# Performance work log

Hardware: AMD Instinct MI355X
Metric: run time of the kernel (lower is better)

The kernel has to match this reference:

```python
import jax, jax.numpy as jnp
import numpy as np
from jax import lax

TEMP = 0.1  # softmax_temp default in forward


def _conv(x, w, b):
    y = lax.conv_general_dilated(x, w, (1, 1), 'VALID',
                                 dimension_numbers=('NCHW', 'OIHW', 'NCHW'))
    return y + b[None, :, None, None]


def _avg_pool2(x):
    # AvgPool2d(2,2), floor mode (VALID window)
    s = lax.reduce_window(x, 0.0, lax.add, (1, 1, 2, 2), (1, 1, 2, 2), 'VALID')
    return s / 4.0


def _cnn(x, c1w, c1b, c2w, c2b, c3w, c3b, dw, db):
    x = _avg_pool2(jax.nn.relu(_conv(x, c1w, c1b)))   # (N,8,13,13)
    x = _avg_pool2(jax.nn.relu(_conv(x, c2w, c2b)))   # (N,16,5,5)
    x = _avg_pool2(jax.nn.relu(_conv(x, c3w, c3b)))   # (N,32,1,1)
    x = x.reshape(x.shape[0], -1)                      # (N,32)
    logits = x @ dw.T + db                             # (N,10)
    return jax.nn.softmax(logits, axis=1)


def _digit_to_rule(p):
    # p: (N,10) -> (N,6)
    return jnp.stack([p[:, 8], p[:, 4] + p[:, 6], p[:, 0] + p[:, 2],
                      p[:, 7] + p[:, 9], p[:, 5], p[:, 1] + p[:, 3]], axis=1)


def setup_inputs() -> dict:
    key = jax.random.key(0)
    ks = jax.random.split(key, 10)
    B, T, D, C, H, W = 256, 8, 4, 1, 28, 28
    sc = 0.1
    return {
        'sequences': jax.random.normal(ks[0], (B, T, D, C, H, W), jnp.float32),
        'conv1_w': jax.random.normal(ks[1], (8, 1, 3, 3), jnp.float32) * sc,
        'conv1_b': jax.random.normal(ks[2], (8,), jnp.float32) * sc,
        'conv2_w': jax.random.normal(ks[3], (16, 8, 3, 3), jnp.float32) * sc,
        'conv2_b': jax.random.normal(ks[4], (16,), jnp.float32) * sc,
        'conv3_w': jax.random.normal(ks[5], (32, 16, 3, 3), jnp.float32) * sc,
        'conv3_b': jax.random.normal(ks[6], (32,), jnp.float32) * sc,
        'dense_w': jax.random.normal(ks[7], (10, 32), jnp.float32) * sc,
        'dense_b': jax.random.normal(ks[8], (10,), jnp.float32) * sc,
        'trans': jax.nn.softmax(jax.random.normal(ks[9], (6, 9, 10), jnp.float32), axis=-1),
    }


def reference(sequences, conv1_w, conv1_b, conv2_w, conv2_b, conv3_w, conv3_b,
              dense_w, dense_b, trans):
    B, T, D, C, H, W = sequences.shape
    S = trans.shape[2]           # num_states = 10
    N = T * D                    # number of recurrence steps
    # CNN is independent per (t,d,b): batch all images at once.
    imgs = jnp.transpose(sequences, (1, 2, 0, 3, 4, 5)).reshape(N * B, C, H, W)
    digit_probs = _cnn(imgs, conv1_w, conv1_b, conv2_w, conv2_b,
                       conv3_w, conv3_b, dense_w, dense_b)      # (N*B,10)
    guard_probs = _digit_to_rule(digit_probs)                   # (N*B,6)

    # Per-rule transition matrices: softmax with temperature + fixed accepting row.
    M = jax.nn.softmax(trans / TEMP, axis=-1)                   # (R,S-1,S)
    acc = jnp.zeros((S,), M.dtype).at[-1].set(1.0)
    M = jnp.concatenate([M, jnp.broadcast_to(acc, (M.shape[0], 1, S))], axis=1)  # (R,S,S)

    # Effective transition matrices per step and batch element.
    g = guard_probs.reshape(N, B, -1)
    A_all = jnp.einsum('nbr,rij->nbij', g, M)                   # (N,B,S,S)

    state0 = jnp.zeros((B, S), sequences.dtype).at[:, 0].set(1.0)

    def step(state, A):
        return jnp.einsum('bi,bij->bj', state, A), None

    state_final, _ = lax.scan(step, state0, A_all)
    all_cnn_preds = digit_probs.reshape(N, B, -1)
    all_guard_preds = g
    return all_cnn_preds, all_guard_preds, state_final
```

## Files before the change

kernel.cpp:

```cpp
#include <hip/hip_runtime.h>

typedef _Float16 half_t;
typedef _Float16 h2 __attribute__((ext_vector_type(2)));
typedef _Float16 h4 __attribute__((ext_vector_type(4)));

__device__ __forceinline__ float fdot2f(h2 a, h2 b, float c) {
#if __has_builtin(__builtin_amdgcn_fdot2)
    return __builtin_amdgcn_fdot2(a, b, c, false);
#else
    return c + (float)a.x * (float)b.x + (float)a.y * (float)b.y;
#endif
}

__global__ __launch_bounds__(256) void prep_kernel(
    const float* __restrict__ w2g, const float* __restrict__ w3g,
    const float* __restrict__ wdg, float* __restrict__ wsW)
{
    const int tid = threadIdx.x;
    half_t* w2h = (half_t*)(wsW + 320);
    half_t* w3h = w2h + 1152;
    for (int i = tid; i < 320; i += 256) {
        int j = i >> 5, c2 = i & 31;
        wsW[c2 * 10 + j] = wdg[i];
    }
    for (int i = tid; i < 1152; i += 256) {
        int l = i & 3, c = (i >> 2) & 15, g = (i >> 6) & 1, k = i >> 7;
        w2h[i] = (half_t)w2g[(c * 8 + g * 4 + l) * 9 + k];
    }
    for (int i = tid; i < 4608; i += 256) {
        int l = i & 3, c = (i >> 2) & 31, g = (i >> 7) & 3, k = i >> 9;
        w3h[i] = (half_t)w3g[(c * 16 + g * 4 + l) * 9 + k];
    }
}

__global__ __launch_bounds__(256, 6) void cnn_kernel(
    const float* __restrict__ seq,
    const float* __restrict__ w1g, const float* __restrict__ b1g,
    const float* __restrict__ b2g, const float* __restrict__ b3g,
    const float* __restrict__ bdg, const float* __restrict__ wsW,
    float* __restrict__ out, float* __restrict__ g_ws)
{
    __shared__ __align__(16) float  s_img2[4][28][28];
    __shared__ __align__(16) half_t s_p1n[4][2][10][11][4];
    __shared__ __align__(16) half_t s_p2n[4][16][16];
    __shared__ float s_p3[4][32];

    const int tid   = threadIdx.x;
    const int mbase = blockIdx.x * 4;
    const float*  wdt = wsW;
    const half_t* w2h = (const half_t*)(wsW + 320);
    const half_t* w3h = w2h + 1152;

    if (tid < 196) {
        #pragma unroll
        for (int img = 0; img < 4; img++) {
            const int m = mbase + img;
            const int b = m & 255, nn = m >> 8;
            const int t = nn >> 2, dd = nn & 3;
            const float4* s4 = (const float4*)(seq + (((size_t)b * 8 + t) * 4 + dd) * 784);
            float4 v = s4[tid];
            int flat = tid * 4;
            int r  = flat / 28;
            int cb = flat - r * 28;
            int e  = cb >> 1;
            *(float2*)&s_img2[img][r][e]      = make_float2(v.x, v.z);
            *(float2*)&s_img2[img][r][14 + e] = make_float2(v.y, v.w);
        }
    }
    __syncthreads();

    for (int idx = tid; idx < 400; idx += 256) {
        const int img = idx / 100;
        const int rem = idx - img * 100;
        const int y   = rem / 10;
        const int x   = rem - y * 10;
        const int r0  = 2 * y;
        float p[4][4];
        #pragma unroll
        for (int i = 0; i < 4; i++) {
            const float* rp = &s_img2[img][r0 + i][0];
            p[i][0] = rp[x];
            p[i][1] = rp[14 + x];
            p[i][2] = rp[x + 1];
            p[i][3] = rp[15 + x];
        }
        float res[8];
        #pragma unroll
        for (int c = 0; c < 8; c++) {
            float w[9];
            #pragma unroll
            for (int k = 0; k < 9; k++) w[k] = w1g[c * 9 + k];
            const float bias = b1g[c];
            float acc = 0.f;
            #pragma unroll
            for (int rr = 0; rr < 2; rr++)
                #pragma unroll
                for (int cc = 0; cc < 2; cc++) {
                    float v = bias;
                    #pragma unroll
                    for (int i = 0; i < 3; i++)
                        #pragma unroll
                        for (int j = 0; j < 3; j++)
                            v += p[rr + i][cc + j] * w[i * 3 + j];
                    acc += fmaxf(v, 0.f);
                }
            res[c] = 0.25f * acc;
        }
        const int slot = (x >> 1) + 5 * (x & 1);
        h4 lo = { (half_t)res[0], (half_t)res[1], (half_t)res[2], (half_t)res[3] };
        h4 hi = { (half_t)res[4], (half_t)res[5], (half_t)res[6], (half_t)res[7] };
        *(h4*)&s_p1n[img][0][y][slot][0] = lo;
        *(h4*)&s_p1n[img][1][y][slot][0] = hi;
    }
    __syncthreads();

    const int img2 = tid >> 6;
    const int t6   = tid & 63;

    {
        const int pos = t6 >> 2;
        const int q   = t6 & 3;
        const int y   = pos >> 2, x = pos & 3;
        const int r0  = 2 * y;
        const int slotm[4] = { x, 5 + x, x + 1, 6 + x };
        float v[4][4];
        #pragma unroll
        for (int oc = 0; oc < 4; oc++) {
            const float bias = b2g[q * 4 + oc];
            #pragma unroll
            for (int w2 = 0; w2 < 4; w2++) v[oc][w2] = bias;
        }
        #pragma unroll
        for (int g = 0; g < 2; g++) {
            h2 aL[4][4], aH[4][4];
            #pragma unroll
            for (int i = 0; i < 4; i++)
                #pragma unroll
                for (int dx = 0; dx < 4; dx++) {
                    h4 a = *(const h4*)&s_p1n[img2][g][r0 + i][slotm[dx]][0];
                    aL[i][dx] = __builtin_shufflevector(a, a, 0, 1);
                    aH[i][dx] = __builtin_shufflevector(a, a, 2, 3);
                }
            #pragma unroll
            for (int oc = 0; oc < 4; oc++) {
                h4 wk[9];
                #pragma unroll
                for (int k = 0; k < 9; k++)
                    wk[k] = *(const h4*)&w2h[((k * 2 + g) * 16 + q * 4 + oc) * 4];
                #pragma unroll
                for (int k = 0; k < 9; k++) {
                    const int di = k / 3, dj = k - di * 3;
                    h2 wL = __builtin_shufflevector(wk[k], wk[k], 0, 1);
                    h2 wH = __builtin_shufflevector(wk[k], wk[k], 2, 3);
                    #pragma unroll
                    for (int rr = 0; rr < 2; rr++)
                        #pragma unroll
                        for (int cc = 0; cc < 2; cc++) {
                            float* acc = &v[oc][rr * 2 + cc];
                            *acc = fdot2f(aL[rr + di][cc + dj], wL, *acc);
                            *acc = fdot2f(aH[rr + di][cc + dj], wH, *acc);
                        }
                }
            }
        }
        float res[4];
        #pragma unroll
        for (int oc = 0; oc < 4; oc++)
            res[oc] = 0.25f * (fmaxf(v[oc][0], 0.f) + fmaxf(v[oc][1], 0.f) +
                               fmaxf(v[oc][2], 0.f) + fmaxf(v[oc][3], 0.f));
        h4 o = { (half_t)res[0], (half_t)res[1], (half_t)res[2], (half_t)res[3] };
        *(h4*)&s_p2n[img2][pos][q * 4] = o;
    }
    __syncthreads();

    {
        const int c = t6 >> 1;
        const int u = t6 & 1;
        float acc0 = b3g[c], acc1 = acc0;
        #pragma unroll
        for (int g = 0; g < 4; g++) {
            h2 AL[3][4], AH[3][4];
            #pragma unroll
            for (int i = 0; i < 3; i++)
                #pragma unroll
                for (int jj = 0; jj < 4; jj++) {
                    h4 a = *(const h4*)&s_p2n[img2][(u + i) * 4 + jj][g * 4];
                    AL[i][jj] = __builtin_shufflevector(a, a, 0, 1);
                    AH[i][jj] = __builtin_shufflevector(a, a, 2, 3);
                }
            h4 wk[9];
            #pragma unroll
            for (int k = 0; k < 9; k++)
                wk[k] = *(const h4*)&w3h[((k * 4 + g) * 32 + c) * 4];
            #pragma unroll
            for (int k = 0; k < 9; k++) {
                const int i = k / 3, j = k - i * 3;
                h2 wL = __builtin_shufflevector(wk[k], wk[k], 0, 1);
                h2 wH = __builtin_shufflevector(wk[k], wk[k], 2, 3);
                acc0 = fdot2f(AL[i][j], wL, acc0);
                acc0 = fdot2f(AH[i][j], wH, acc0);
                acc1 = fdot2f(AL[i][j + 1], wL, acc1);
                acc1 = fdot2f(AH[i][j + 1], wH, acc1);
            }
        }
        float s = fmaxf(acc0, 0.f) + fmaxf(acc1, 0.f);
        s += __shfl_xor(s, 1, 64);
        if (u == 0) s_p3[img2][c] = 0.25f * s;
    }
    __syncthreads();

    {
        float logit = -1e30f;
        if (t6 < 10) {
            float acc = bdg[t6];
            #pragma unroll
            for (int c2 = 0; c2 < 32; c2++) acc += s_p3[img2][c2] * wdt[c2 * 10 + t6];
            logit = acc;
        }
        float mx = logit;
        #pragma unroll
        for (int s = 1; s < 16; s <<= 1) mx = fmaxf(mx, __shfl_xor(mx, s, 16));
        float e = (t6 < 10) ? __expf(logit - mx) : 0.f;
        float ssum = e;
        #pragma unroll
        for (int s = 1; s < 16; s <<= 1) ssum += __shfl_xor(ssum, s, 16);
        float p = e / ssum;
        const int m = mbase + img2;
        if (t6 < 10) out[(size_t)m * 10 + t6] = p;

        const int sh = (t6 < 6 ? t6 : 0) * 4;
        const int ia = (0x157048 >> sh) & 0xF;
        const int ib = (0x3F926F >> sh) & 0xF;
        float pa = __shfl(p, ia, 16);
        float pb = __shfl(p, ib, 16);
        if (t6 < 6) {
            float gv = pa + pb;
            out[81920 + (size_t)m * 6 + t6] = gv;
            g_ws[(size_t)m * 6 + t6] = gv;
        }
    }
}

__global__ __launch_bounds__(256) void sfa_kernel(
    const float* __restrict__ trans,
    const float* __restrict__ g_ws,
    float* __restrict__ out)
{
    __shared__ float M[600];
    const int tid  = threadIdx.x;
    const int lane = tid & 63;
    const int wv   = tid >> 6;

    if (tid < 54) {
        int r = tid / 9, i = tid - r * 9;
        const float* row = trans + (size_t)(r * 9 + i) * 10;
        float x[10], mx = -1e30f;
        #pragma unroll
        for (int j = 0; j < 10; j++) { x[j] = 10.f * row[j]; mx = fmaxf(mx, x[j]); }
        float s = 0.f;
        #pragma unroll
        for (int j = 0; j < 10; j++) { x[j] = __expf(x[j] - mx); s += x[j]; }
        float inv = 1.f / s;
        #pragma unroll
        for (int j = 0; j < 10; j++) M[(r * 9 + i) * 10 + j] = x[j] * inv;
    }
    __syncthreads();

    const int bb    = lane / 10;
    const int j     = lane - bb * 10;
    const int base  = bb * 10;
    const bool ok   = (bb < 6);
    int batch = blockIdx.x * 24 + wv * 6 + bb;
    const bool live = ok && (batch < 256);
    if (!live) batch = 0;

    float Mreg[54];
    #pragma unroll
    for (int k = 0; k < 54; k++) Mreg[k] = M[k * 10 + j];

    float stj = (j == 0) ? 1.f : 0.f;

    for (int nn = 0; nn < 32; nn++) {
        const float* gp = g_ws + ((size_t)nn * 256 + batch) * 6;
        float2 ga = *(const float2*)(gp);
        float2 gb = *(const float2*)(gp + 2);
        float2 gc = *(const float2*)(gp + 4);
        float g[6] = {ga.x, ga.y, gb.x, gb.y, gc.x, gc.y};

        float st[10];
        #pragma unroll
        for (int i = 0; i < 10; i++) st[i] = __shfl(stj, base + i, 64);

        float gsum = g[0] + g[1] + g[2] + g[3] + g[4] + g[5];
        float ns = (j == 9) ? gsum * st[9] : 0.f;
        #pragma unroll
        for (int r = 0; r < 6; r++) {
            float h = 0.f;
            #pragma unroll
            for (int i = 0; i < 9; i++) h += st[i] * Mreg[r * 9 + i];
            ns += g[r] * h;
        }
        stj = ns;
    }
    if (live) out[131072 + (size_t)batch * 10 + j] = stj;
}

extern "C" void kernel_launch(void* const* d_in, const int* in_sizes, int n_in,
                              void* d_out, int out_size, void* d_ws, size_t ws_size,
                              hipStream_t stream) {
    const float* seq = (const float*)d_in[0];
    const float* w1  = (const float*)d_in[1];
    const float* b1  = (const float*)d_in[2];
    const float* w2  = (const float*)d_in[3];
    const float* b2  = (const float*)d_in[4];
    const float* w3  = (const float*)d_in[5];
    const float* b3  = (const float*)d_in[6];
    const float* wd  = (const float*)d_in[7];
    const float* bd  = (const float*)d_in[8];
    const float* tr  = (const float*)d_in[9];
    float* out  = (float*)d_out;
    float* g_ws = (float*)d_ws;
    float* wsW  = g_ws + 49152;

    prep_kernel<<<1, 256, 0, stream>>>(w2, w3, wd, wsW);
    cnn_kernel<<<2048, 256, 0, stream>>>(seq, w1, b1, b2, b3, bd, wsW, out, g_ws);
    sfa_kernel<<<11, 256, 0, stream>>>(tr, g_ws, out);
}
```

Baseline: 138.6 us.

## Double CNN block threads and split channel work; drop duplicate guard workspace

The CNN kernel now launches 512 threads per block for the same four images. Each stage's channel work is split across twice as many threads: conv1 by output-channel half, conv2 by channel pairs, and conv3 by input-group halves combined with a shuffle. The goal is more parallelism and latency hiding per block, at the cost of higher register pressure and more idle threads in the dense/softmax stage. The redundant guard-probability write to workspace is also removed, and the SFA kernel now reads guards directly from the output buffer.

Measured after the change: 154.9 us. 11.7% more time.

```diff
diff --git a/kernel.cpp b/kernel.cpp
--- a/kernel.cpp
+++ b/kernel.cpp
@@ -33,12 +33,12 @@
     }
 }
 
-__global__ __launch_bounds__(256, 6) void cnn_kernel(
+__global__ __launch_bounds__(512, 6) void cnn_kernel(
     const float* __restrict__ seq,
     const float* __restrict__ w1g, const float* __restrict__ b1g,
     const float* __restrict__ b2g, const float* __restrict__ b3g,
     const float* __restrict__ bdg, const float* __restrict__ wsW,
-    float* __restrict__ out, float* __restrict__ g_ws)
+    float* __restrict__ out)
 {
     __shared__ __align__(16) float  s_img2[4][28][28];
     __shared__ __align__(16) half_t s_p1n[4][2][10][11][4];
@@ -51,15 +51,17 @@
     const half_t* w2h = (const half_t*)(wsW + 320);
     const half_t* w3h = w2h + 1152;
 
-    if (tid < 196) {
-        #pragma unroll
-        for (int img = 0; img < 4; img++) {
-            const int m = mbase + img;
-            const int b = m & 255, nn = m >> 8;
-            const int t = nn >> 2, dd = nn & 3;
-            const float4* s4 = (const float4*)(seq + (((size_t)b * 8 + t) * 4 + dd) * 784);
-            float4 v = s4[tid];
-            int flat = tid * 4;
+    const int img = tid >> 7;
+    const int t7  = tid & 127;
+
+    {
+        const int m = mbase + img;
+        const int b = m & 255, nn = m >> 8;
+        const int t = nn >> 2, dd = nn & 3;
+        const float4* s4 = (const float4*)(seq + (((size_t)b * 8 + t) * 4 + dd) * 784);
+        for (int i = t7; i < 196; i += 128) {
+            float4 v = s4[i];
+            int flat = i * 4;
             int r  = flat / 28;
             int cb = flat - r * 28;
             int e  = cb >> 1;
@@ -69,24 +71,27 @@
     }
     __syncthreads();
 
-    for (int idx = tid; idx < 400; idx += 256) {
-        const int img = idx / 100;
-        const int rem = idx - img * 100;
-        const int y   = rem / 10;
-        const int x   = rem - y * 10;
+    for (int idx = tid; idx < 800; idx += 512) {
+        const int im  = idx / 200;
+        const int rem = idx - im * 200;
+        const int och = rem / 100;
+        const int pp  = rem - och * 100;
+        const int y   = pp / 10;
+        const int x   = pp - y * 10;
         const int r0  = 2 * y;
         float p[4][4];
         #pragma unroll
         for (int i = 0; i < 4; i++) {
-            const float* rp = &s_img2[img][r0 + i][0];
+            const float* rp = &s_img2[im][r0 + i][0];
             p[i][0] = rp[x];
             p[i][1] = rp[14 + x];
             p[i][2] = rp[x + 1];
             p[i][3] = rp[15 + x];
         }
-        float res[8];
-        #pragma unroll
-        for (int c = 0; c < 8; c++) {
+        float res[4];
+        #pragma unroll
+        for (int cl = 0; cl < 4; cl++) {
+            const int c = och * 4 + cl;
             float w[9];
             #pragma unroll
             for (int k = 0; k < 9; k++) w[k] = w1g[c * 9 + k];
@@ -104,31 +109,26 @@
                             v += p[rr + i][cc + j] * w[i * 3 + j];
                     acc += fmaxf(v, 0.f);
                 }
-            res[c] = 0.25f * acc;
+            res[cl] = 0.25f * acc;
         }
         const int slot = (x >> 1) + 5 * (x & 1);
-        h4 lo = { (half_t)res[0], (half_t)res[1], (half_t)res[2], (half_t)res[3] };
-        h4 hi = { (half_t)res[4], (half_t)res[5], (half_t)res[6], (half_t)res[7] };
-        *(h4*)&s_p1n[img][0][y][slot][0] = lo;
-        *(h4*)&s_p1n[img][1][y][slot][0] = hi;
-    }
-    __syncthreads();
-
-    const int img2 = tid >> 6;
-    const int t6   = tid & 63;
+        h4 o = { (half_t)res[0], (half_t)res[1], (half_t)res[2], (half_t)res[3] };
+        *(h4*)&s_p1n[im][och][y][slot][0] = o;
+    }
+    __syncthreads();
 
     {
-        const int pos = t6 >> 2;
-        const int q   = t6 & 3;
+        const int pos = t7 >> 3;
+        const int q2  = t7 & 7;
         const int y   = pos >> 2, x = pos & 3;
         const int r0  = 2 * y;
         const int slotm[4] = { x, 5 + x, x + 1, 6 + x };
-        float v[4][4];
-        #pragma unroll
-        for (int oc = 0; oc < 4; oc++) {
-            const float bias = b2g[q * 4 + oc];
-            #pragma unroll
-            for (int w2 = 0; w2 < 4; w2++) v[oc][w2] = bias;
+        float v[2][4];
+        #pragma unroll
+        for (int ocl = 0; ocl < 2; ocl++) {
+            const float bias = b2g[q2 * 2 + ocl];
+            #pragma unroll
+            for (int w2 = 0; w2 < 4; w2++) v[ocl][w2] = bias;
         }
         #pragma unroll
         for (int g = 0; g < 2; g++) {
@@ -137,16 +137,17 @@
             for (int i = 0; i < 4; i++)
                 #pragma unroll
                 for (int dx = 0; dx < 4; dx++) {
-                    h4 a = *(const h4*)&s_p1n[img2][g][r0 + i][slotm[dx]][0];
+                    h4 a = *(const h4*)&s_p1n[img][g][r0 + i][slotm[dx]][0];
                     aL[i][dx] = __builtin_shufflevector(a, a, 0, 1);
                     aH[i][dx] = __builtin_shufflevector(a, a, 2, 3);
                 }
             #pragma unroll
-            for (int oc = 0; oc < 4; oc++) {
+            for (int ocl = 0; ocl < 2; ocl++) {
+                const int oc = q2 * 2 + ocl;
                 h4 wk[9];
                 #pragma unroll
                 for (int k = 0; k < 9; k++)
-                    wk[k] = *(const h4*)&w2h[((k * 2 + g) * 16 + q * 4 + oc) * 4];
+                    wk[k] = *(const h4*)&w2h[((k * 2 + g) * 16 + oc) * 4];
                 #pragma unroll
                 for (int k = 0; k < 9; k++) {
                     const int di = k / 3, dj = k - di * 3;
@@ -156,35 +157,37 @@
                     for (int rr = 0; rr < 2; rr++)
                         #pragma unroll
                         for (int cc = 0; cc < 2; cc++) {
-                            float* acc = &v[oc][rr * 2 + cc];
+                            float* acc = &v[ocl][rr * 2 + cc];
                             *acc = fdot2f(aL[rr + di][cc + dj], wL, *acc);
                             *acc = fdot2f(aH[rr + di][cc + dj], wH, *acc);
                         }
                 }
             }
         }
-        float res[4];
-        #pragma unroll
-        for (int oc = 0; oc < 4; oc++)
-            res[oc] = 0.25f * (fmaxf(v[oc][0], 0.f) + fmaxf(v[oc][1], 0.f) +
-                               fmaxf(v[oc][2], 0.f) + fmaxf(v[oc][3], 0.f));
-        h4 o = { (half_t)res[0], (half_t)res[1], (half_t)res[2], (half_t)res[3] };
-        *(h4*)&s_p2n[img2][pos][q * 4] = o;
+        float r0v = 0.25f * (fmaxf(v[0][0], 0.f) + fmaxf(v[0][1], 0.f) +
+                             fmaxf(v[0][2], 0.f) + fmaxf(v[0][3], 0.f));
+        float r1v = 0.25f * (fmaxf(v[1][0], 0.f) + fmaxf(v[1][1], 0.f) +
+                             fmaxf(v[1][2], 0.f) + fmaxf(v[1][3], 0.f));
+        h2 o = { (half_t)r0v, (half_t)r1v };
+        *(h2*)&s_p2n[img][pos][q2 * 2] = o;
     }
     __syncthreads();
 
     {
-        const int c = t6 >> 1;
-        const int u = t6 & 1;
-        float acc0 = b3g[c], acc1 = acc0;
-        #pragma unroll
-        for (int g = 0; g < 4; g++) {
+        const int c  = t7 >> 2;
+        const int u  = (t7 >> 1) & 1;
+        const int gh = t7 & 1;
+        float acc0 = (gh == 0) ? b3g[c] : 0.f;
+        float acc1 = acc0;
+        #pragma unroll
+        for (int gg = 0; gg < 2; gg++) {
+            const int g = gh * 2 + gg;
             h2 AL[3][4], AH[3][4];
             #pragma unroll
             for (int i = 0; i < 3; i++)
                 #pragma unroll
                 for (int jj = 0; jj < 4; jj++) {
-                    h4 a = *(const h4*)&s_p2n[img2][(u + i) * 4 + jj][g * 4];
+                    h4 a = *(const h4*)&s_p2n[img][(u + i) * 4 + jj][g * 4];
                     AL[i][jj] = __builtin_shufflevector(a, a, 0, 1);
                     AH[i][jj] = __builtin_shufflevector(a, a, 2, 3);
                 }
@@ -203,18 +206,21 @@
                 acc1 = fdot2f(AH[i][j + 1], wH, acc1);
             }
         }
+        acc0 += __shfl_xor(acc0, 1, 64);
+        acc1 += __shfl_xor(acc1, 1, 64);
         float s = fmaxf(acc0, 0.f) + fmaxf(acc1, 0.f);
-        s += __shfl_xor(s, 1, 64);
-        if (u == 0) s_p3[img2][c] = 0.25f * s;
-    }
-    __syncthreads();
-
-    {
+        s += __shfl_xor(s, 2, 64);
+        if ((t7 & 3) == 0) s_p3[img][c] = 0.25f * s;
+    }
+    __syncthreads();
+
+    if (((tid >> 6) & 1) == 0) {
+        const int t6 = tid & 63;
         float logit = -1e30f;
         if (t6 < 10) {
             float acc = bdg[t6];
             #pragma unroll
-            for (int c2 = 0; c2 < 32; c2++) acc += s_p3[img2][c2] * wdt[c2 * 10 + t6];
+            for (int c2 = 0; c2 < 32; c2++) acc += s_p3[img][c2] * wdt[c2 * 10 + t6];
             logit = acc;
         }
         float mx = logit;
@@ -225,7 +231,7 @@
         #pragma unroll
         for (int s = 1; s < 16; s <<= 1) ssum += __shfl_xor(ssum, s, 16);
         float p = e / ssum;
-        const int m = mbase + img2;
+        const int m = mbase + img;
         if (t6 < 10) out[(size_t)m * 10 + t6] = p;
 
         const int sh = (t6 < 6 ? t6 : 0) * 4;
@@ -233,17 +239,14 @@
         const int ib = (0x3F926F >> sh) & 0xF;
         float pa = __shfl(p, ia, 16);
         float pb = __shfl(p, ib, 16);
-        if (t6 < 6) {
-            float gv = pa + pb;
-            out[81920 + (size_t)m * 6 + t6] = gv;
-            g_ws[(size_t)m * 6 + t6] = gv;
-        }
+        if (t6 < 6)
+            out[81920 + (size_t)m * 6 + t6] = pa + pb;
     }
 }
 
 __global__ __launch_bounds__(256) void sfa_kernel(
     const float* __restrict__ trans,
-    const float* __restrict__ g_ws,
+    const float* __restrict__ out_guards,
     float* __restrict__ out)
 {
     __shared__ float M[600];
@@ -279,9 +282,10 @@
     for (int k = 0; k < 54; k++) Mreg[k] = M[k * 10 + j];
 
     float stj = (j == 0) ? 1.f : 0.f;
+    const float* gbase = out_guards + 81920;
 
     for (int nn = 0; nn < 32; nn++) {
-        const float* gp = g_ws + ((size_t)nn * 256 + batch) * 6;
+        const float* gp = gbase + ((size_t)nn * 256 + batch) * 6;
         float2 ga = *(const float2*)(gp);
         float2 gb = *(const float2*)(gp + 2);
         float2 gc = *(const float2*)(gp + 4);
@@ -318,11 +322,10 @@
     const float* wd  = (const float*)d_in[7];
     const float* bd  = (const float*)d_in[8];
     const float* tr  = (const float*)d_in[9];
-    float* out  = (float*)d_out;
-    float* g_ws = (float*)d_ws;
-    float* wsW  = g_ws + 49152;
+    float* out = (float*)d_out;
+    float* wsW = (float*)d_ws;
 
     prep_kernel<<<1, 256, 0, stream>>>(w2, w3, wd, wsW);
-    cnn_kernel<<<2048, 256, 0, stream>>>(seq, w1, b1, b2, b3, bd, wsW, out, g_ws);
-    sfa_kernel<<<11, 256, 0, stream>>>(tr, g_ws, out);
-}
+    cnn_kernel<<<2048, 512, 0, stream>>>(seq, w1, b1, b2, b3, bd, wsW, out);
+    sfa_kernel<<<11, 256, 0, stream>>>(tr, out, out);
+}
```
